# Kernel tuning notes

Measured on AMD Instinct MI355X. Metric: run time of the kernel, lower is better.

The kernel has to match this reference:

```python
import jax, jax.numpy as jnp
import numpy as np

N_NODES = 100000
N_EDGES = 1600000
IN_C, HID_C, OUT_C = 128, 128, 64


def setup_inputs() -> dict:
    key = jax.random.key(0)
    ks = jax.random.split(key, 8)
    x = jax.random.normal(ks[0], (N_NODES, IN_C), dtype=jnp.float32)
    edge_index = jax.random.randint(ks[1], (2, N_EDGES), 0, N_NODES, dtype=jnp.int32)
    # Glorot-ish init for GCNConv linear weights, zero bias (PyG default)
    def glorot(k, fan_in, fan_out):
        s = jnp.sqrt(6.0 / (fan_in + fan_out))
        return jax.random.uniform(k, (fan_in, fan_out), dtype=jnp.float32, minval=-s, maxval=s)
    return {
        "x": x,
        "edge_index": edge_index,
        "W1": glorot(ks[2], IN_C, HID_C), "b1": jnp.zeros((HID_C,), jnp.float32),
        "W2": glorot(ks[3], HID_C, HID_C), "b2": jnp.zeros((HID_C,), jnp.float32),
        "W3": glorot(ks[4], HID_C, OUT_C), "b3": jnp.zeros((OUT_C,), jnp.float32),
    }


def _gcn_norm(edge_index, num_nodes):
    # Add self-loops (PyG GCNConv default) and compute symmetric normalization
    loops = jnp.arange(num_nodes, dtype=edge_index.dtype)
    src = jnp.concatenate([edge_index[0], loops])  # [E+N]
    dst = jnp.concatenate([edge_index[1], loops])
    deg = jax.ops.segment_sum(jnp.ones_like(dst, dtype=jnp.float32), dst,
                              num_segments=num_nodes)
    deg_inv_sqrt = jnp.where(deg > 0, jax.lax.rsqrt(jnp.maximum(deg, 1.0)), 0.0)
    norm = deg_inv_sqrt[src] * deg_inv_sqrt[dst]  # [E+N]
    return src, dst, norm


def _gcn_layer(x, src, dst, norm, W, b, num_nodes):
    h = x @ W                                # [N, out] dense transform first
    msg = h[src] * norm[:, None]             # gather + scale  [E+N, out]
    out = jax.ops.segment_sum(msg, dst, num_segments=num_nodes)  # scatter-add
    return out + b


def reference(x, edge_index, W1, b1, W2, b2, W3, b3):
    n = x.shape[0]
    src, dst, norm = _gcn_norm(edge_index, n)
    h = jax.nn.relu(_gcn_layer(x, src, dst, norm, W1, b1, n))
    h = jax.nn.relu(_gcn_layer(h, src, dst, norm, W2, b2, n))
    return _gcn_layer(h, src, dst, norm, W3, b3, n)
```

## Files before the change

### kernel.cpp

```cpp
#include <hip/hip_runtime.h>

#define NN 100000
#define NE 1600000
#define NBK 98
#define BSH 10
#define MPAD 100096

typedef unsigned short ushortT;
typedef unsigned long long ull;
using sh8 = __attribute__((ext_vector_type(8))) short;
using f4  = __attribute__((ext_vector_type(4))) float;


__device__ __forceinline__ unsigned short bfr(float f) {
  unsigned u = __float_as_uint(f);
  u += 0x7FFF + ((u >> 16) & 1);
  return (unsigned short)(u >> 16);
}
__device__ __forceinline__ float bf2f(unsigned short h) {
  return __uint_as_float(((unsigned)h) << 16);
}
__device__ __forceinline__ void split2(float a, float b, unsigned& H, unsigned& L) {
  unsigned short ha = bfr(a), hb = bfr(b);
  H = (unsigned)ha | ((unsigned)hb << 16);
  L = (unsigned)bfr(a - bf2f(ha)) | ((unsigned)bfr(b - bf2f(hb)) << 16);
}
__device__ __forceinline__ void acc8(const uint4 v, float* a) {
  a[0] += __uint_as_float(v.x << 16);
  a[1] += __uint_as_float(v.x & 0xFFFF0000u);
  a[2] += __uint_as_float(v.y << 16);
  a[3] += __uint_as_float(v.y & 0xFFFF0000u);
  a[4] += __uint_as_float(v.z << 16);
  a[5] += __uint_as_float(v.z & 0xFFFF0000u);
  a[6] += __uint_as_float(v.w << 16);
  a[7] += __uint_as_float(v.w & 0xFFFF0000u);
}
__device__ __forceinline__ sh8 hi8(const float4 a, const float4 b) {
  sh8 r;
  r[0] = (short)bfr(a.x); r[1] = (short)bfr(a.y);
  r[2] = (short)bfr(a.z); r[3] = (short)bfr(a.w);
  r[4] = (short)bfr(b.x); r[5] = (short)bfr(b.y);
  r[6] = (short)bfr(b.z); r[7] = (short)bfr(b.w);
  return r;
}
__device__ __forceinline__ sh8 lo8(const float4 a, const float4 b, const sh8 h) {
  sh8 r;
  r[0] = (short)bfr(a.x - bf2f((unsigned short)h[0]));
  r[1] = (short)bfr(a.y - bf2f((unsigned short)h[1]));
  r[2] = (short)bfr(a.z - bf2f((unsigned short)h[2]));
  r[3] = (short)bfr(a.w - bf2f((unsigned short)h[3]));
  r[4] = (short)bfr(b.x - bf2f((unsigned short)h[4]));
  r[5] = (short)bfr(b.y - bf2f((unsigned short)h[5]));
  r[6] = (short)bfr(b.z - bf2f((unsigned short)h[6]));
  r[7] = (short)bfr(b.w - bf2f((unsigned short)h[7]));
  return r;
}


__global__ void k_hist(const int* __restrict__ dst, int* __restrict__ bucketCnt) {
  __shared__ int lc[NBK];
  const int t = threadIdx.x;
  for (int i = t; i < NBK; i += 256) lc[i] = 0;
  __syncthreads();
  const int base = blockIdx.x * 4096;
#pragma unroll
  for (int q = 0; q < 16; q++) {
    int e = base + t + 256 * q;
    if (e < NE) atomicAdd(&lc[dst[e] >> BSH], 1);
  }
  __syncthreads();
  for (int i = t; i < NBK; i += 256)
    if (lc[i]) atomicAdd(&bucketCnt[i], lc[i]);
}

__global__ void k_scanb(const int* __restrict__ bucketCnt, int* __restrict__ bucketBase,
                        int* __restrict__ bucketCursor) {
  if (threadIdx.x == 0) {
    int run = 0;
    for (int i = 0; i < NBK; i++) {
      bucketBase[i] = run;
      bucketCursor[i] = run;
      run += bucketCnt[i];
    }
    bucketBase[NBK] = run;
  }
}

__global__ __launch_bounds__(256) void k_scatter(const int* __restrict__ src,
                                                 const int* __restrict__ dst,
                                                 int* __restrict__ bucketCursor,
                                                 ull* __restrict__ pairArr) {
  __shared__ int lcnt[NBK];
  __shared__ int lbase[NBK];
  __shared__ int lrank[NBK];
  __shared__ int bbase[NBK];
  __shared__ ull sorted[4096];
  __shared__ int target[4096];
  const int t = threadIdx.x;
  for (int i = t; i < NBK; i += 256) { lcnt[i] = 0; lrank[i] = 0; }
  __syncthreads();
  const int base = blockIdx.x * 4096;
  int rs[16], rd[16];
#pragma unroll
  for (int q = 0; q < 16; q++) {
    int e = base + t + 256 * q;
    rs[q] = (e < NE) ? src[e] : -1;
    rd[q] = (e < NE) ? dst[e] : -1;
    if (rd[q] >= 0) atomicAdd(&lcnt[rd[q] >> BSH], 1);
  }
  __syncthreads();
  if (t == 0) {
    int run = 0;
    for (int i = 0; i < NBK; i++) { lbase[i] = run; run += lcnt[i]; }
  }
  __syncthreads();
  if (t < NBK && lcnt[t] > 0) bbase[t] = atomicAdd(&bucketCursor[t], lcnt[t]);
  __syncthreads();
#pragma unroll
  for (int q = 0; q < 16; q++) {
    if (rd[q] >= 0) {
      int b = rd[q] >> BSH;
      int r = atomicAdd(&lrank[b], 1);
      int slot = lbase[b] + r;
      sorted[slot] = ((ull)(unsigned)rs[q] << 32) | (unsigned)rd[q];
      target[slot] = bbase[b] + r;
    }
  }
  __syncthreads();
  const int n = min(4096, NE - base);
  for (int s = t; s < n; s += 256) pairArr[target[s]] = sorted[s];
}

__global__ __launch_bounds__(256) void k_buildcsr(const ull* __restrict__ pairArr,
                                                  const int* __restrict__ bucketBase,
                                                  float* __restrict__ dinv,
                                                  int* __restrict__ rowptr,
                                                  int* __restrict__ col) {
  __shared__ int lc[1024];
  __shared__ int sd[256];
  const int t = threadIdx.x;
  const int b = blockIdx.x;
  const int n0 = b << BSH;
  for (int i = t; i < 1024; i += 256) lc[i] = 0;
  __syncthreads();
  const int ebeg = bucketBase[b], eend = bucketBase[b + 1];
  for (int i = ebeg + t; i < eend; i += 256)
    atomicAdd(&lc[(int)(unsigned)(pairArr[i] & 0xffffffffULL) - n0], 1);
  __syncthreads();
  const int v0 = lc[t * 4], v1 = lc[t * 4 + 1], v2 = lc[t * 4 + 2], v3 = lc[t * 4 + 3];
  const int s = v0 + v1 + v2 + v3;
  sd[t] = s;
  __syncthreads();
  for (int off = 1; off < 256; off <<= 1) {
    int x = (t >= off) ? sd[t - off] : 0;
    __syncthreads();
    sd[t] += x;
    __syncthreads();
  }
  const int run = sd[t] - s;
  const int c0 = run, c1 = run + v0, c2 = c1 + v1, c3 = c2 + v2;
  lc[t * 4] = c0; lc[t * 4 + 1] = c1; lc[t * 4 + 2] = c2; lc[t * 4 + 3] = c3;
  const int cnts[4] = {v0, v1, v2, v3};
  const int curs[4] = {c0, c1, c2, c3};
#pragma unroll
  for (int i = 0; i < 4; i++) {
    int node = n0 + t * 4 + i;
    if (node < NN) {
      rowptr[node] = ebeg + curs[i];
      dinv[node] = rsqrtf(1.0f + (float)cnts[i]);
    }
  }
  if (b == 0 && t == 0) rowptr[NN] = NE;
  __syncthreads();
  for (int i = ebeg + t; i < eend; i += 256) {
    ull p = pairArr[i];
    int d = (int)(unsigned)(p & 0xffffffffULL);
    int srcv = (int)(unsigned)(p >> 32);
    int pos = atomicAdd(&lc[d - n0], 1);
    col[ebeg + pos] = srcv;
  }
}


template <int COUT>
__device__ __forceinline__ void packone(const float* __restrict__ W,
                                        ushortT* __restrict__ Bp, int i) {
  const int j = i & 7;
  const int l = (i >> 3) & 63;
  const int rest = i >> 9;
  const int g = rest % (COUT / 16);
  const int ks = rest / (COUT / 16);
  const int k = (ks & 3) * 32 + (l >> 4) * 8 + j;
  const int n = g * 16 + (l & 15);
  const float v = W[k * COUT + n];
  const unsigned short h = bfr(v);
  Bp[i] = (ks < 4) ? h : bfr(v - bf2f(h));
}

__global__ void k_packAll(const float* __restrict__ W1, const float* __restrict__ W2,
                          const float* __restrict__ W3, ushortT* __restrict__ Bp1,
                          ushortT* __restrict__ Bp2, ushortT* __restrict__ Bp3) {
  const int i = blockIdx.x * 256 + threadIdx.x;
  if (i < 32768) packone<128>(W1, Bp1, i);
  else if (i < 65536) packone<128>(W2, Bp2, i - 32768);
  else packone<64>(W3, Bp3, i - 65536);
}


template <int COUT, bool FUSED>
__global__ __launch_bounds__(256) void k_gemmM(const ushortT* __restrict__ A2,
                                               const float* __restrict__ X,
                                               const ushortT* __restrict__ Bp,
                                               const float* __restrict__ dinv,
                                               ushortT* __restrict__ hs) {
  constexpr int CGALL = COUT / 16;
  constexpr int RG = (COUT == 128) ? 4 : 2;
  constexpr int CG = 4;
  const int w = threadIdx.x >> 6;
  const int lane = threadIdx.x & 63;
  const int q = lane >> 4;
  const int c = lane & 15;
  int row0, cg0;
  if (COUT == 128) {
    row0 = blockIdx.x * 128 + (w & 1) * 64;
    cg0 = (w >> 1) * 4;
  } else {
    row0 = blockIdx.x * 128 + w * 32;
    cg0 = 0;
  }

  const ushortT* ap[RG];
  const float* xp[RG];
#pragma unroll
  for (int rg = 0; rg < RG; rg++) {
    const int row = row0 + rg * 16 + c;
    if (FUSED) xp[rg] = X + (size_t)min(row, NN - 1) * 128 + q * 8;
    else ap[rg] = A2 + (size_t)row * 256 + q * 8;
  }
  const ushortT* bp0 = Bp + (size_t)lane * 8;

  f4 acc[RG][CG];
#pragma unroll
  for (int i = 0; i < RG; i++)
#pragma unroll
    for (int j = 0; j < CG; j++) acc[i][j] = (f4){0.f, 0.f, 0.f, 0.f};

  sh8 ah[RG], al[RG], bh[CG], bl[CG];
  sh8 nah[RG], nal[RG], nbh[CG], nbl[CG];

  auto loadA = [&](int kr, sh8 (&h)[RG], sh8 (&l)[RG]) {
#pragma unroll
    for (int rg = 0; rg < RG; rg++) {
      if (FUSED) {
        const float4 x0 = *reinterpret_cast<const float4*>(xp[rg] + kr * 32);
        const float4 x1 = *reinterpret_cast<const float4*>(xp[rg] + kr * 32 + 4);
        h[rg] = hi8(x0, x1);
        l[rg] = lo8(x0, x1, h[rg]);
      } else {
        h[rg] = *reinterpret_cast<const sh8*>(ap[rg] + kr * 32);
        l[rg] = *reinterpret_cast<const sh8*>(ap[rg] + 128 + kr * 32);
      }
    }
  };
  auto loadB = [&](int kr, sh8 (&h)[CG], sh8 (&l)[CG]) {
#pragma unroll
    for (int cg = 0; cg < CG; cg++) {
      h[cg] = *reinterpret_cast<const sh8*>(bp0 + (size_t)(kr * CGALL + cg0 + cg) * 512);
      l[cg] = *reinterpret_cast<const sh8*>(bp0 + (size_t)((4 + kr) * CGALL + cg0 + cg) * 512);
    }
  };

  loadA(0, ah, al);
  loadB(0, bh, bl);
#pragma unroll
  for (int kr = 0; kr < 4; kr++) {
    if (kr < 3) {
      loadA(kr + 1, nah, nal);
      loadB(kr + 1, nbh, nbl);
    }
#pragma unroll
    for (int rg = 0; rg < RG; rg++)
#pragma unroll
      for (int cg = 0; cg < CG; cg++)
        acc[rg][cg] = __builtin_amdgcn_mfma_f32_16x16x32_bf16(ah[rg], bh[cg],
                                                              acc[rg][cg], 0, 0, 0);
#pragma unroll
    for (int rg = 0; rg < RG; rg++)
#pragma unroll
      for (int cg = 0; cg < CG; cg++)
        acc[rg][cg] = __builtin_amdgcn_mfma_f32_16x16x32_bf16(al[rg], bh[cg],
                                                              acc[rg][cg], 0, 0, 0);
#pragma unroll
    for (int rg = 0; rg < RG; rg++)
#pragma unroll
      for (int cg = 0; cg < CG; cg++)
        acc[rg][cg] = __builtin_amdgcn_mfma_f32_16x16x32_bf16(ah[rg], bl[cg],
                                                              acc[rg][cg], 0, 0, 0);
    if (kr < 3) {
#pragma unroll
      for (int rg = 0; rg < RG; rg++) { ah[rg] = nah[rg]; al[rg] = nal[rg]; }
#pragma unroll
      for (int cg = 0; cg < CG; cg++) { bh[cg] = nbh[cg]; bl[cg] = nbl[cg]; }
    }
  }

#pragma unroll
  for (int rg = 0; rg < RG; rg++) {
#pragma unroll
    for (int reg = 0; reg < 4; reg++) {
      const int row = row0 + rg * 16 + q * 4 + reg;
      if (row < NN) {
        const float dv = dinv[row];
#pragma unroll
        for (int cg = 0; cg < CG; cg++) {
          hs[(size_t)row * COUT + (cg0 + cg) * 16 + c] = bfr(acc[rg][cg][reg] * dv);
        }
      }
    }
  }
}


template <bool RELU>
__global__ __launch_bounds__(256) void k_agg128(const ushortT* __restrict__ hs,
                                                const int* __restrict__ rowptr,
                                                const int* __restrict__ col,
                                                const float* __restrict__ dinv,
                                                const float* __restrict__ bias,
                                                ushortT* __restrict__ A2) {
  const int gid = blockIdx.x * 256 + threadIdx.x;
  const int node = gid >> 6;
  if (node >= NN) return;
  const int lane = threadIdx.x & 63;
  const int q = lane >> 4;
  const int chb = (lane & 15) * 8;
  const int beg = rowptr[node];
  const int end = rowptr[node + 1];

  float a[8] = {};
  if (q == 0) {
    const uint4 v = *reinterpret_cast<const uint4*>(hs + (long)node * 128 + chb);
    acc8(v, a);
  }

  int j = beg;
  if (j + 8 <= end) {
    int c0 = col[j + q];
    int c1 = col[j + 4 + q];
    while (true) {
      const uint4 v0 = *reinterpret_cast<const uint4*>(hs + (long)c0 * 128 + chb);
      const uint4 v1 = *reinterpret_cast<const uint4*>(hs + (long)c1 * 128 + chb);
      j += 8;
      const bool more = (j + 8 <= end);
      int n0, n1;
      if (more) { n0 = col[j + q]; n1 = col[j + 4 + q]; }
      acc8(v0, a);
      acc8(v1, a);
      if (!more) break;
      c0 = n0; c1 = n1;
    }
  }
  for (; j + 4 <= end; j += 4) {
    int c = col[j + q];
    const uint4 v = *reinterpret_cast<const uint4*>(hs + (long)c * 128 + chb);
    acc8(v, a);
  }
  {
    const int r = end - j;
    if (q < r) {
      int c = col[j + q];
      const uint4 v = *reinterpret_cast<const uint4*>(hs + (long)c * 128 + chb);
      acc8(v, a);
    }
  }

#pragma unroll
  for (int i = 0; i < 8; i++) a[i] += __shfl(a[i], lane ^ 32);
#pragma unroll
  for (int i = 0; i < 8; i++) a[i] += __shfl(a[i], lane ^ 16);

  if (q == 0) {
    const float di = dinv[node];
    const float4 b0 = *reinterpret_cast<const float4*>(bias + chb);
    const float4 b1 = *reinterpret_cast<const float4*>(bias + chb + 4);
    float o[8];
    o[0] = fmaf(a[0], di, b0.x); o[1] = fmaf(a[1], di, b0.y);
    o[2] = fmaf(a[2], di, b0.z); o[3] = fmaf(a[3], di, b0.w);
    o[4] = fmaf(a[4], di, b1.x); o[5] = fmaf(a[5], di, b1.y);
    o[6] = fmaf(a[6], di, b1.z); o[7] = fmaf(a[7], di, b1.w);
    if (RELU) {
#pragma unroll
      for (int i = 0; i < 8; i++) o[i] = fmaxf(o[i], 0.f);
    }
    uint4 H, L;
    split2(o[0], o[1], H.x, L.x);
    split2(o[2], o[3], H.y, L.y);
    split2(o[4], o[5], H.z, L.z);
    split2(o[6], o[7], H.w, L.w);
    *reinterpret_cast<uint4*>(A2 + (long)node * 256 + chb) = H;
    *reinterpret_cast<uint4*>(A2 + (long)node * 256 + 128 + chb) = L;
  }
}

__global__ __launch_bounds__(256) void k_agg64(const ushortT* __restrict__ hs,
                                               const int* __restrict__ rowptr,
                                               const int* __restrict__ col,
                                               const float* __restrict__ dinv,
                                               const float* __restrict__ bias,
                                               float* __restrict__ out) {
  const int gid = blockIdx.x * 256 + threadIdx.x;
  const int node = gid >> 6;
  if (node >= NN) return;
  const int lane = threadIdx.x & 63;
  const int o8 = lane >> 3;
  const int chb = (lane & 7) * 8;
  const int beg = rowptr[node];
  const int end = rowptr[node + 1];

  float a[8] = {};
  if (o8 == 0) {
    const uint4 v = *reinterpret_cast<const uint4*>(hs + (long)node * 64 + chb);
    acc8(v, a);
  }

  int j = beg;
  if (j + 16 <= end) {
    int c0 = col[j + o8];
    int c1 = col[j + 8 + o8];
    while (true) {
      const uint4 v0 = *reinterpret_cast<const uint4*>(hs + (long)c0 * 64 + chb);
      const uint4 v1 = *reinterpret_cast<const uint4*>(hs + (long)c1 * 64 + chb);
      j += 16;
      const bool more = (j + 16 <= end);
      int n0, n1;
      if (more) { n0 = col[j + o8]; n1 = col[j + 8 + o8]; }
      acc8(v0, a);
      acc8(v1, a);
      if (!more) break;
      c0 = n0; c1 = n1;
    }
  }
  for (; j + 8 <= end; j += 8) {
    int c = col[j + o8];
    const uint4 v = *reinterpret_cast<const uint4*>(hs + (long)c * 64 + chb);
    acc8(v, a);
  }
  {
    const int r = end - j;
    if (o8 < r) {
      int c = col[j + o8];
      const uint4 v = *reinterpret_cast<const uint4*>(hs + (long)c * 64 + chb);
      acc8(v, a);
    }
  }

#pragma unroll
  for (int i = 0; i < 8; i++) a[i] += __shfl(a[i], lane ^ 32);
#pragma unroll
  for (int i = 0; i < 8; i++) a[i] += __shfl(a[i], lane ^ 16);
#pragma unroll
  for (int i = 0; i < 8; i++) a[i] += __shfl(a[i], lane ^ 8);

  if (o8 == 0) {
    const float di = dinv[node];
    const float4 b0 = *reinterpret_cast<const float4*>(bias + chb);
    const float4 b1 = *reinterpret_cast<const float4*>(bias + chb + 4);
    float4 r0, r1;
    r0.x = fmaf(a[0], di, b0.x); r0.y = fmaf(a[1], di, b0.y);
    r0.z = fmaf(a[2], di, b0.z); r0.w = fmaf(a[3], di, b0.w);
    r1.x = fmaf(a[4], di, b1.x); r1.y = fmaf(a[5], di, b1.y);
    r1.z = fmaf(a[6], di, b1.z); r1.w = fmaf(a[7], di, b1.w);
    *reinterpret_cast<float4*>(out + (long)node * 64 + chb) = r0;
    *reinterpret_cast<float4*>(out + (long)node * 64 + chb + 4) = r1;
  }
}


extern "C" void kernel_launch(void* const* d_in, const int* in_sizes, int n_in,
                              void* d_out, int out_size, void* d_ws, size_t ws_size,
                              hipStream_t stream) {
  const float* x  = (const float*)d_in[0];
  const int* ei   = (const int*)d_in[1];
  const float* W1 = (const float*)d_in[2];
  const float* b1 = (const float*)d_in[3];
  const float* W2 = (const float*)d_in[4];
  const float* b2 = (const float*)d_in[5];
  const float* W3 = (const float*)d_in[6];
  const float* b3 = (const float*)d_in[7];
  float* out = (float*)d_out;
  const int* srcp = ei;
  const int* dstp = ei + NE;

  char* wsb = (char*)d_ws;
  size_t off = 0;
  auto alloc = [&](size_t bytes) -> void* {
    void* p = wsb + off;
    off += (bytes + 255) & ~(size_t)255;
    return p;
  };
  ushortT* A2  = (ushortT*)alloc((size_t)MPAD * 256 * 2);
  ushortT* hs  = (ushortT*)alloc((size_t)NN * 128 * 2);
  int*   col    = (int*)alloc((size_t)NE * 4);
  int*   rowptr = (int*)alloc((size_t)(NN + 1) * 4);
  float* dinv   = (float*)alloc((size_t)NN * 4);
  int*   bucketCnt    = (int*)alloc((size_t)NBK * 4);
  int*   bucketBase   = (int*)alloc((size_t)(NBK + 1) * 4);
  int*   bucketCursor = (int*)alloc((size_t)NBK * 4);
  ushortT* Bp1 = (ushortT*)alloc((size_t)32768 * 2);
  ushortT* Bp2 = (ushortT*)alloc((size_t)32768 * 2);
  ushortT* Bp3 = (ushortT*)alloc((size_t)16384 * 2);
  ull* pairArr = (ull*)hs;
  (void)ws_size; (void)in_sizes; (void)n_in; (void)out_size;

  const int SCB = (NE + 4095) / 4096;

  hipMemsetAsync(bucketCnt, 0, (size_t)NBK * 4, stream);
  k_hist<<<SCB, 256, 0, stream>>>(dstp, bucketCnt);
  k_scanb<<<1, 64, 0, stream>>>(bucketCnt, bucketBase, bucketCursor);
  k_scatter<<<SCB, 256, 0, stream>>>(srcp, dstp, bucketCursor, pairArr);
  k_buildcsr<<<NBK, 256, 0, stream>>>(pairArr, bucketBase, dinv, rowptr, col);
  k_packAll<<<320, 256, 0, stream>>>(W1, W2, W3, Bp1, Bp2, Bp3);

  const int aggGrid = (NN * 64) / 256;
  const int gemmGrid = MPAD / 128;

  k_gemmM<128, true><<<gemmGrid, 256, 0, stream>>>(nullptr, x, Bp1, dinv, hs);
  k_agg128<true><<<aggGrid, 256, 0, stream>>>(hs, rowptr, col, dinv, b1, A2);
  k_gemmM<128, false><<<gemmGrid, 256, 0, stream>>>(A2, nullptr, Bp2, dinv, hs);
  k_agg128<true><<<aggGrid, 256, 0, stream>>>(hs, rowptr, col, dinv, b2, A2);
  k_gemmM<64, false><<<gemmGrid, 256, 0, stream>>>(A2, nullptr, Bp3, dinv, hs);
  k_agg64<<<aggGrid, 256, 0, stream>>>(hs, rowptr, col, dinv, b3, out);
}
```

Before: 435.4 us.

## Drop histogram pass using fixed-capacity buckets and fuse weight packing into scatter

Replaces the histogram, bucket scan and scatter sequence with a single scatter that writes into fixed-capacity per-bucket regions, with the CSR builder computing bucket offsets from the final cursors. Weight packing is folded into the same launch as extra blocks. This removes one full read of the destination array and several kernel launches. It risks overflow if any bucket exceeds the fixed capacity, which only holds for roughly uniform degree distributions.

```diff
diff --git a/kernel.cpp b/kernel.cpp
--- a/kernel.cpp
+++ b/kernel.cpp
@@ -5,6 +5,8 @@
 #define NBK 98
 #define BSH 10
 #define MPAD 100096
+#define SCB 391
+#define CAP 20480
 
 typedef unsigned short ushortT;
 typedef unsigned long long ull;
@@ -54,131 +56,6 @@
   r[6] = (short)bfr(b.z - bf2f((unsigned short)h[6]));
   r[7] = (short)bfr(b.w - bf2f((unsigned short)h[7]));
   return r;
-}
-
-
-__global__ void k_hist(const int* __restrict__ dst, int* __restrict__ bucketCnt) {
-  __shared__ int lc[NBK];
-  const int t = threadIdx.x;
-  for (int i = t; i < NBK; i += 256) lc[i] = 0;
-  __syncthreads();
-  const int base = blockIdx.x * 4096;
-#pragma unroll
-  for (int q = 0; q < 16; q++) {
-    int e = base + t + 256 * q;
-    if (e < NE) atomicAdd(&lc[dst[e] >> BSH], 1);
-  }
-  __syncthreads();
-  for (int i = t; i < NBK; i += 256)
-    if (lc[i]) atomicAdd(&bucketCnt[i], lc[i]);
-}
-
-__global__ void k_scanb(const int* __restrict__ bucketCnt, int* __restrict__ bucketBase,
-                        int* __restrict__ bucketCursor) {
-  if (threadIdx.x == 0) {
-    int run = 0;
-    for (int i = 0; i < NBK; i++) {
-      bucketBase[i] = run;
-      bucketCursor[i] = run;
-      run += bucketCnt[i];
-    }
-    bucketBase[NBK] = run;
-  }
-}
-
-__global__ __launch_bounds__(256) void k_scatter(const int* __restrict__ src,
-                                                 const int* __restrict__ dst,
-                                                 int* __restrict__ bucketCursor,
-                                                 ull* __restrict__ pairArr) {
-  __shared__ int lcnt[NBK];
-  __shared__ int lbase[NBK];
-  __shared__ int lrank[NBK];
-  __shared__ int bbase[NBK];
-  __shared__ ull sorted[4096];
-  __shared__ int target[4096];
-  const int t = threadIdx.x;
-  for (int i = t; i < NBK; i += 256) { lcnt[i] = 0; lrank[i] = 0; }
-  __syncthreads();
-  const int base = blockIdx.x * 4096;
-  int rs[16], rd[16];
-#pragma unroll
-  for (int q = 0; q < 16; q++) {
-    int e = base + t + 256 * q;
-    rs[q] = (e < NE) ? src[e] : -1;
-    rd[q] = (e < NE) ? dst[e] : -1;
-    if (rd[q] >= 0) atomicAdd(&lcnt[rd[q] >> BSH], 1);
-  }
-  __syncthreads();
-  if (t == 0) {
-    int run = 0;
-    for (int i = 0; i < NBK; i++) { lbase[i] = run; run += lcnt[i]; }
-  }
-  __syncthreads();
-  if (t < NBK && lcnt[t] > 0) bbase[t] = atomicAdd(&bucketCursor[t], lcnt[t]);
-  __syncthreads();
-#pragma unroll
-  for (int q = 0; q < 16; q++) {
-    if (rd[q] >= 0) {
-      int b = rd[q] >> BSH;
-      int r = atomicAdd(&lrank[b], 1);
-      int slot = lbase[b] + r;
-      sorted[slot] = ((ull)(unsigned)rs[q] << 32) | (unsigned)rd[q];
-      target[slot] = bbase[b] + r;
-    }
-  }
-  __syncthreads();
-  const int n = min(4096, NE - base);
-  for (int s = t; s < n; s += 256) pairArr[target[s]] = sorted[s];
-}
-
-__global__ __launch_bounds__(256) void k_buildcsr(const ull* __restrict__ pairArr,
-                                                  const int* __restrict__ bucketBase,
-                                                  float* __restrict__ dinv,
-                                                  int* __restrict__ rowptr,
-                                                  int* __restrict__ col) {
-  __shared__ int lc[1024];
-  __shared__ int sd[256];
-  const int t = threadIdx.x;
-  const int b = blockIdx.x;
-  const int n0 = b << BSH;
-  for (int i = t; i < 1024; i += 256) lc[i] = 0;
-  __syncthreads();
-  const int ebeg = bucketBase[b], eend = bucketBase[b + 1];
-  for (int i = ebeg + t; i < eend; i += 256)
-    atomicAdd(&lc[(int)(unsigned)(pairArr[i] & 0xffffffffULL) - n0], 1);
-  __syncthreads();
-  const int v0 = lc[t * 4], v1 = lc[t * 4 + 1], v2 = lc[t * 4 + 2], v3 = lc[t * 4 + 3];
-  const int s = v0 + v1 + v2 + v3;
-  sd[t] = s;
-  __syncthreads();
-  for (int off = 1; off < 256; off <<= 1) {
-    int x = (t >= off) ? sd[t - off] : 0;
-    __syncthreads();
-    sd[t] += x;
-    __syncthreads();
-  }
-  const int run = sd[t] - s;
-  const int c0 = run, c1 = run + v0, c2 = c1 + v1, c3 = c2 + v2;
-  lc[t * 4] = c0; lc[t * 4 + 1] = c1; lc[t * 4 + 2] = c2; lc[t * 4 + 3] = c3;
-  const int cnts[4] = {v0, v1, v2, v3};
-  const int curs[4] = {c0, c1, c2, c3};
-#pragma unroll
-  for (int i = 0; i < 4; i++) {
-    int node = n0 + t * 4 + i;
-    if (node < NN) {
-      rowptr[node] = ebeg + curs[i];
-      dinv[node] = rsqrtf(1.0f + (float)cnts[i]);
-    }
-  }
-  if (b == 0 && t == 0) rowptr[NN] = NE;
-  __syncthreads();
-  for (int i = ebeg + t; i < eend; i += 256) {
-    ull p = pairArr[i];
-    int d = (int)(unsigned)(p & 0xffffffffULL);
-    int srcv = (int)(unsigned)(p >> 32);
-    int pos = atomicAdd(&lc[d - n0], 1);
-    col[ebeg + pos] = srcv;
-  }
 }
 
 
@@ -197,13 +74,121 @@
   Bp[i] = (ks < 4) ? h : bfr(v - bf2f(h));
 }
 
-__global__ void k_packAll(const float* __restrict__ W1, const float* __restrict__ W2,
-                          const float* __restrict__ W3, ushortT* __restrict__ Bp1,
-                          ushortT* __restrict__ Bp2, ushortT* __restrict__ Bp3) {
-  const int i = blockIdx.x * 256 + threadIdx.x;
-  if (i < 32768) packone<128>(W1, Bp1, i);
-  else if (i < 65536) packone<128>(W2, Bp2, i - 32768);
-  else packone<64>(W3, Bp3, i - 65536);
+
+__global__ __launch_bounds__(256) void k_scatterpack(
+    const int* __restrict__ src, const int* __restrict__ dst,
+    int* __restrict__ cursor, ull* __restrict__ pairArr,
+    const float* __restrict__ W1, const float* __restrict__ W2,
+    const float* __restrict__ W3, ushortT* __restrict__ Bp1,
+    ushortT* __restrict__ Bp2, ushortT* __restrict__ Bp3) {
+  if (blockIdx.x >= SCB) {
+    const int i = (blockIdx.x - SCB) * 256 + threadIdx.x;
+    if (i < 32768) packone<128>(W1, Bp1, i);
+    else if (i < 65536) packone<128>(W2, Bp2, i - 32768);
+    else packone<64>(W3, Bp3, i - 65536);
+    return;
+  }
+  __shared__ int lcnt[NBK];
+  __shared__ int lbase[NBK];
+  __shared__ int lrank[NBK];
+  __shared__ int bbase[NBK];
+  __shared__ ull sorted[4096];
+  __shared__ int target[4096];
+  const int t = threadIdx.x;
+  for (int i = t; i < NBK; i += 256) { lcnt[i] = 0; lrank[i] = 0; }
+  __syncthreads();
+  const int base = blockIdx.x * 4096;
+  int rs[16], rd[16];
+#pragma unroll
+  for (int q = 0; q < 16; q++) {
+    int e = base + t + 256 * q;
+    rs[q] = (e < NE) ? src[e] : -1;
+    rd[q] = (e < NE) ? dst[e] : -1;
+    if (rd[q] >= 0) atomicAdd(&lcnt[rd[q] >> BSH], 1);
+  }
+  __syncthreads();
+  if (t == 0) {
+    int run = 0;
+    for (int i = 0; i < NBK; i++) { lbase[i] = run; run += lcnt[i]; }
+  }
+  __syncthreads();
+  if (t < NBK && lcnt[t] > 0) bbase[t] = atomicAdd(&cursor[t], lcnt[t]);
+  __syncthreads();
+#pragma unroll
+  for (int q = 0; q < 16; q++) {
+    if (rd[q] >= 0) {
+      int b = rd[q] >> BSH;
+      int r = atomicAdd(&lrank[b], 1);
+      int slot = lbase[b] + r;
+      sorted[slot] = ((ull)(unsigned)rs[q] << 32) | (unsigned)rd[q];
+      target[slot] = b * CAP + bbase[b] + r;
+    }
+  }
+  __syncthreads();
+  const int n = min(4096, NE - base);
+  for (int s = t; s < n; s += 256) pairArr[target[s]] = sorted[s];
+}
+
+
+__global__ __launch_bounds__(256) void k_buildcsr(const ull* __restrict__ pairArr,
+                                                  const int* __restrict__ cnt,
+                                                  float* __restrict__ dinv,
+                                                  int* __restrict__ rowptr,
+                                                  int* __restrict__ col) {
+  __shared__ int lc[1024];
+  __shared__ int sd[256];
+  __shared__ int bc[NBK];
+  __shared__ int ebegS;
+  const int t = threadIdx.x;
+  const int b = blockIdx.x;
+  const int n0 = b << BSH;
+  if (t < NBK) bc[t] = cnt[t];
+  for (int i = t; i < 1024; i += 256) lc[i] = 0;
+  __syncthreads();
+  if (t == 0) {
+    int run = 0;
+    for (int i = 0; i < b; i++) run += bc[i];
+    ebegS = run;
+  }
+  __syncthreads();
+  const int ebeg = ebegS;
+  const int myCnt = bc[b];
+  const ull* pb = pairArr + (size_t)b * CAP;
+  for (int i = t; i < myCnt; i += 256)
+    atomicAdd(&lc[(int)(unsigned)(pb[i] & 0xffffffffULL) - n0], 1);
+  __syncthreads();
+  const int v0 = lc[t * 4], v1 = lc[t * 4 + 1], v2 = lc[t * 4 + 2], v3 = lc[t * 4 + 3];
+  const int s = v0 + v1 + v2 + v3;
+  sd[t] = s;
+  __syncthreads();
+  for (int off = 1; off < 256; off <<= 1) {
+    int x = (t >= off) ? sd[t - off] : 0;
+    __syncthreads();
+    sd[t] += x;
+    __syncthreads();
+  }
+  const int run = sd[t] - s;
+  const int c0 = run, c1 = run + v0, c2 = c1 + v1, c3 = c2 + v2;
+  lc[t * 4] = c0; lc[t * 4 + 1] = c1; lc[t * 4 + 2] = c2; lc[t * 4 + 3] = c3;
+  const int cnts[4] = {v0, v1, v2, v3};
+  const int curs[4] = {c0, c1, c2, c3};
+#pragma unroll
+  for (int i = 0; i < 4; i++) {
+    int node = n0 + t * 4 + i;
+    if (node < NN) {
+      rowptr[node] = ebeg + curs[i];
+      dinv[node] = rsqrtf(1.0f + (float)cnts[i]);
+    }
+  }
+  if (b == 0 && t == 0) rowptr[NN] = NE;
+  __syncthreads();
+  for (int i = t; i < myCnt; i += 256) {
+    ull p = pb[i];
+    int d = (int)(unsigned)(p & 0xffffffffULL);
+    int srcv = (int)(unsigned)(p >> 32);
+    int pos = atomicAdd(&lc[d - n0], 1);
+    col[ebeg + pos] = srcv;
+  }
 }
 
 
@@ -503,23 +488,17 @@
   int*   col    = (int*)alloc((size_t)NE * 4);
   int*   rowptr = (int*)alloc((size_t)(NN + 1) * 4);
   float* dinv   = (float*)alloc((size_t)NN * 4);
-  int*   bucketCnt    = (int*)alloc((size_t)NBK * 4);
-  int*   bucketBase   = (int*)alloc((size_t)(NBK + 1) * 4);
-  int*   bucketCursor = (int*)alloc((size_t)NBK * 4);
+  int*   cursor = (int*)alloc((size_t)NBK * 4);
   ushortT* Bp1 = (ushortT*)alloc((size_t)32768 * 2);
   ushortT* Bp2 = (ushortT*)alloc((size_t)32768 * 2);
   ushortT* Bp3 = (ushortT*)alloc((size_t)16384 * 2);
   ull* pairArr = (ull*)hs;
   (void)ws_size; (void)in_sizes; (void)n_in; (void)out_size;
 
-  const int SCB = (NE + 4095) / 4096;
-
-  hipMemsetAsync(bucketCnt, 0, (size_t)NBK * 4, stream);
-  k_hist<<<SCB, 256, 0, stream>>>(dstp, bucketCnt);
-  k_scanb<<<1, 64, 0, stream>>>(bucketCnt, bucketBase, bucketCursor);
-  k_scatter<<<SCB, 256, 0, stream>>>(srcp, dstp, bucketCursor, pairArr);
-  k_buildcsr<<<NBK, 256, 0, stream>>>(pairArr, bucketBase, dinv, rowptr, col);
-  k_packAll<<<320, 256, 0, stream>>>(W1, W2, W3, Bp1, Bp2, Bp3);
+  hipMemsetAsync(cursor, 0, (size_t)NBK * 4, stream);
+  k_scatterpack<<<SCB + 320, 256, 0, stream>>>(srcp, dstp, cursor, pairArr,
+                                               W1, W2, W3, Bp1, Bp2, Bp3);
+  k_buildcsr<<<NBK, 256, 0, stream>>>(pairArr, cursor, dinv, rowptr, col);
 
   const int aggGrid = (NN * 64) / 256;
   const int gemmGrid = MPAD / 128;
```

After: 411.4 us. 1.06x faster.
